# Performance work log

Measured on AMD Instinct MI355X. Metric: run time of the kernel, lower is better.

Reference implementation:

```python
import jax, jax.numpy as jnp
import numpy as np

B, S, K, D, H, F = 2, 2048, 2048, 1024, 16, 4096
HD = D // H
LN_EPS = 1e-5  # nn.LayerNorm default (module's eps arg is unused by the norms)


def setup_inputs() -> dict:
    key = jax.random.key(0)
    ks = jax.random.split(key, 12)
    def w(k, shape, scale=0.02):
        return jax.random.normal(k, shape, jnp.float32) * scale
    return {
        "x": jax.random.normal(ks[0], (B, S, D), jnp.float32),
        "context": jax.random.normal(ks[1], (B, K, D), jnp.float32),
        "Wq": w(ks[2], (D, D)), "bq": jnp.zeros((D,), jnp.float32),
        "Wk": w(ks[3], (D, D)), "bk": jnp.zeros((D,), jnp.float32),
        "Wv": w(ks[4], (D, D)), "bv": jnp.zeros((D,), jnp.float32),
        "W1": w(ks[5], (F, D)), "b1": jnp.zeros((F,), jnp.float32),
        "W2": w(ks[6], (D, F)), "b2": jnp.zeros((D,), jnp.float32),
        "g1": jnp.ones((D,), jnp.float32), "be1": jnp.zeros((D,), jnp.float32),
        "g2": jnp.ones((D,), jnp.float32), "be2": jnp.zeros((D,), jnp.float32),
    }


def _ln(x, g, b):
    m = jnp.mean(x, axis=-1, keepdims=True)
    v = jnp.var(x, axis=-1, keepdims=True)
    return (x - m) / jnp.sqrt(v + LN_EPS) * g + b


def _split_heads(t, L):
    # [B, L, D] -> [B, H, L, HD]
    return t.reshape(B, L, H, HD).transpose(0, 2, 1, 3)


def reference(x, context, Wq, bq, Wk, bk, Wv, bv, W1, b1, W2, b2, g1, be1, g2, be2):
    q = _split_heads(x @ Wq.T + bq, S)
    k = _split_heads(context @ Wk.T + bk, K)
    v = _split_heads(context @ Wv.T + bv, K)
    # NOTE: original scales by sqrt(encoder_out_dim), not sqrt(head_dim)
    scores = jnp.einsum('bhqd,bhkd->bhqk', q, k) / jnp.sqrt(jnp.float32(D))
    attn = jax.nn.softmax(scores, axis=-1)
    ctx = jnp.einsum('bhqk,bhkd->bhqd', attn, v)
    # faithful to original: raw reshape of [B,H,S,HD] -> [B,S,D] (no head transpose)
    out1 = ctx.reshape(B, S, D)
    out1 = x + _ln(out1, g1, be1)
    h = jax.nn.gelu(out1 @ W1.T + b1, approximate=False)
    out2 = _ln(h @ W2.T + b2, g2, be2)
    return out1 + out2
```

## Files before the change

kernel.cpp:

```cpp
#include <hip/hip_runtime.h>
#include <hip/hip_bf16.h>

#define BB 2
#define SS 2048
#define KK 2048
#define DD 1024
#define HH 16
#define FF 4096

using bf16x8 = __attribute__((ext_vector_type(8))) __bf16;
using f32x4  = __attribute__((ext_vector_type(4))) float;
using u16 = unsigned short;

__device__ __forceinline__ float bf2f(u16 u){
  union { unsigned int i; float f; } c; c.i = ((unsigned int)u) << 16; return c.f;
}
__device__ __forceinline__ u16 f2bf(float f){
  union { float f; unsigned int i; } c; c.f = f;
  return (u16)((c.i + 0x7fffu + ((c.i >> 16) & 1u)) >> 16);
}
__device__ __forceinline__ float gelu_exact(float x){
  return 0.5f * x * (1.f + erff(x * 0.70710678118654752f));
}

__device__ __forceinline__ void gll16(const void* g, const void* l) {
  __builtin_amdgcn_global_load_lds(
      (const __attribute__((address_space(1))) void*)(unsigned long long)(size_t)g,
      (__attribute__((address_space(3))) void*)(unsigned int)(size_t)l,
      16, 0, 0);
}

#define E_X   0
#define E_CX  4194304
#define E_WQ  8388608
#define E_BQ  9437184
#define E_WK  9438208
#define E_BK  10486784
#define E_WV  10487808
#define E_BV  11536384
#define E_W1  11537408
#define E_B1  15731712
#define E_W2  15735808
#define E_B2  19930112
#define E_G1  19931136
#define E_BE1 19932160
#define E_G2  19933184
#define E_BE2 19934208
#define E_TOT 19935232

struct Ptrs { const void* p[16]; };

__global__ __launch_bounds__(256)
void convert_inputs(Ptrs ptrs, u16* __restrict__ dst)
{
  const bool is_f32 = (((const u16*)ptrs.p[12])[0] == 0);
  const int szs[16] = {4194304, 4194304, 1048576, 1024, 1048576, 1024,
                       1048576, 1024, 4194304, 4096, 4194304, 1024,
                       1024, 1024, 1024, 1024};
  long long gbase = (long long)blockIdx.x * 1024;
  int seg = 0; long long start = 0;
  while (seg < 15 && gbase >= start + szs[seg]) { start += szs[seg]; seg++; }
  const long long local = gbase - start;
  const int tid = threadIdx.x;
  u16 outv[4];
  if (is_f32) {
    const float4* s = (const float4*)((const float*)ptrs.p[seg] + local);
    float4 v = s[tid];
    outv[0] = f2bf(v.x); outv[1] = f2bf(v.y); outv[2] = f2bf(v.z); outv[3] = f2bf(v.w);
  } else {
    const uint2* s = (const uint2*)((const u16*)ptrs.p[seg] + local);
    uint2 v = s[tid];
    *(uint2*)outv = v;
  }
  *(uint2*)(dst + gbase + (long long)tid * 4) = *(uint2*)outv;
}

template<int EPI>
__device__ __forceinline__
void gemm256_core(const u16* __restrict__ A, const u16* __restrict__ W,
                  const u16* __restrict__ bias, void* __restrict__ Cout,
                  int N, int Kd, int lda, int n0, int m0, u16* lds)
{
  const int tid = threadIdx.x;
  const int wv = tid >> 6, lane = tid & 63;
  const int wm = wv >> 2, wn = wv & 3;
  const int l16 = lane & 15, quad = lane >> 4;
  const int sw = (quad ^ ((l16 >> 1) & 3)) * 8;

  const int aRdOff = (wm * 128 + l16) * 32 + sw;
  const int bRdOff = (wn * 64 + l16) * 32 + sw;

  const int rA0 = wm * 128 + wn * 32 + (lane >> 2);
  const int rB0 = (wn >> 1) * 128 + (wm * 2 + (wn & 1)) * 32 + (lane >> 2);
  const u16* gA = A + (size_t)(m0 + rA0) * lda + (((lane & 3) ^ ((rA0 >> 1) & 3)) * 8);
  const u16* gB = W + (size_t)(n0 + rB0) * lda + (((lane & 3) ^ ((rB0 >> 1) & 3)) * 8);
  const int aStBase = (wm * 128 + wn * 32) * 32;
  const int bStBase = ((wn >> 1) * 128 + (wm * 2 + (wn & 1)) * 32) * 32;
  const size_t rs16 = (size_t)16 * lda;

  f32x4 acc[8][4] = {};

  auto stage4 = [&](int nbo, int kc, int ktn) {
    const u16* ga = gA + ktn + kc * 32;
    const u16* gb = gB + ktn + kc * 32;
    u16* la = lds + nbo + kc * 8192 + aStBase;
    u16* lb = lds + nbo + 16384 + kc * 8192 + bStBase;
    gll16(ga, la); gll16(ga + rs16, la + 512);
    gll16(gb, lb); gll16(gb + rs16, lb + 512);
  };

  auto interval = [&](int bo, int nbo, int kc, int ktn) {
    asm volatile("s_waitcnt vmcnt(4)" ::: "memory");
    __builtin_amdgcn_s_barrier();
    asm volatile("" ::: "memory");
    stage4(nbo, kc, ktn);
    const u16* Ab = lds + bo + kc * 8192;
    const u16* Bb = Ab + 16384;
    bf16x8 bfr[4], afr[4];
#pragma unroll
    for (int j = 0; j < 4; ++j) bfr[j] = *(const bf16x8*)(Bb + bRdOff + j * 512);
#pragma unroll
    for (int i = 0; i < 4; ++i) afr[i] = *(const bf16x8*)(Ab + aRdOff + i * 512);
    __builtin_amdgcn_s_setprio(1);
#pragma unroll
    for (int i = 0; i < 4; ++i)
#pragma unroll
      for (int j = 0; j < 4; ++j)
        acc[i][j] = __builtin_amdgcn_mfma_f32_16x16x32_bf16(afr[i], bfr[j], acc[i][j], 0, 0, 0);
    __builtin_amdgcn_s_setprio(0);
#pragma unroll
    for (int i = 0; i < 4; ++i) afr[i] = *(const bf16x8*)(Ab + aRdOff + (4 + i) * 512);
    __builtin_amdgcn_s_setprio(1);
#pragma unroll
    for (int i = 0; i < 4; ++i)
#pragma unroll
      for (int j = 0; j < 4; ++j)
        acc[4 + i][j] = __builtin_amdgcn_mfma_f32_16x16x32_bf16(afr[i], bfr[j], acc[4 + i][j], 0, 0, 0);
    __builtin_amdgcn_s_setprio(0);
  };

  stage4(0, 0, 0);
  stage4(0, 1, 0);

  const int NT = Kd >> 6;
#pragma unroll 1
  for (int t = 0; t < NT; t += 2) {
    const int kt1 = ((t + 1 < NT) ? t + 1 : t) << 6;
    interval(0, 32768, 0, kt1);
    interval(0, 32768, 1, kt1);
    const int kt2 = ((t + 2 < NT) ? t + 2 : t + 1) << 6;
    interval(32768, 0, 0, kt2);
    interval(32768, 0, 1, kt2);
  }

#pragma unroll
  for (int i = 0; i < 8; i++)
#pragma unroll
    for (int j = 0; j < 4; j++) {
      const int mb = m0 + wm * 128 + 16 * i + quad * 4;
      const int n  = n0 + wn * 64 + 16 * j + l16;
      if (EPI == 5) {
#pragma unroll
        for (int r = 0; r < 4; r++)
          ((u16*)Cout)[(size_t)(mb + r) * N + n] = f2bf(acc[i][j][r]);
      } else {
        const float bv = bf2f(bias[n]);
        if (EPI == 3) {
          u16 pk[4];
#pragma unroll
          for (int r = 0; r < 4; r++) pk[r] = f2bf(acc[i][j][r] + bv);
          const int b = mb >> 11, key = mb & 2047;
          *(uint2*)((u16*)Cout + ((size_t)((b * HH + (n >> 6)) * 64 + (n & 63))) * KK + key)
              = *(uint2*)pk;
        } else {
#pragma unroll
          for (int r = 0; r < 4; r++) {
            float vv = acc[i][j][r] + bv;
            if (EPI == 1) vv = gelu_exact(vv);
            ((u16*)Cout)[(size_t)(mb + r) * N + n] = f2bf(vv);
          }
        }
      }
    }
}

template<int EPI>
__global__ __launch_bounds__(512, 2)
void gemm256(const u16* __restrict__ A, const u16* __restrict__ W,
             const u16* __restrict__ bias, void* __restrict__ Cout,
             int N, int Kd, int lda)
{
  __shared__ u16 lds[65536];
  gemm256_core<EPI>(A, W, bias, Cout, N, Kd, lda,
                    blockIdx.x * 256, blockIdx.y * 256, lds);
}

__global__ __launch_bounds__(512, 2)
void qkv_gemm256(const u16* __restrict__ conv, u16* __restrict__ q_ws,
                 u16* __restrict__ k_ws, u16* __restrict__ vt_ws)
{
  __shared__ u16 lds[65536];
  const int n0 = blockIdx.x * 256, m0 = blockIdx.y * 256;
  const int z = blockIdx.z;
  if (z == 0)
    gemm256_core<0>(conv + E_X,  conv + E_WQ, conv + E_BQ, q_ws,  DD, DD, DD, n0, m0, lds);
  else if (z == 1)
    gemm256_core<0>(conv + E_CX, conv + E_WK, conv + E_BK, k_ws,  DD, DD, DD, n0, m0, lds);
  else
    gemm256_core<3>(conv + E_CX, conv + E_WV, conv + E_BV, vt_ws, DD, DD, DD, n0, m0, lds);
}

__global__ __launch_bounds__(512, 2)
void ffn2_gemm256(const u16* __restrict__ h, const u16* __restrict__ W2,
                  u16* __restrict__ pa, u16* __restrict__ pb,
                  u16* __restrict__ pc, u16* __restrict__ pd)
{
  __shared__ u16 lds[65536];
  u16* outs[4] = {pa, pb, pc, pd};
  const int z = blockIdx.z;
  gemm256_core<5>(h + (size_t)z * 1024, W2 + (size_t)z * 1024, nullptr, outs[z],
                  DD, 1024, FF, blockIdx.x * 256, blockIdx.y * 256, lds);
}

#define ATT_SCALE 0.03125f

__global__ __launch_bounds__(512, 4)
void attn_flash(const u16* __restrict__ q, const u16* __restrict__ k,
                const u16* __restrict__ vt, const u16* __restrict__ x,
                const u16* __restrict__ g1, const u16* __restrict__ be1,
                u16* __restrict__ o1)
{
  __shared__ u16 Qs[128 * 64];
  __shared__ u16 Ks0[64 * 64], Ks1[64 * 64];
  __shared__ u16 Vt0[64 * 64], Vt1[64 * 64];
  __shared__ u16 Ps[8][16 * 72];
  const int tid = threadIdx.x, wv = tid >> 6, lane = tid & 63;
  const int l16 = lane & 15, quad = lane >> 4;
  const int s0 = blockIdx.x * 128;
  const int bh = blockIdx.y, b = bh >> 4, h = bh & 15;
  const size_t qgbase = ((size_t)b * SS + s0) * DD + h * 64;
  const size_t kgbase = (size_t)b * KK * DD + h * 64;
  const size_t vtbase = (size_t)bh * 64 * KK;
  const int srow = tid >> 3, sc8 = tid & 7;
  const int c8s = sc8 ^ (srow & 7);

  auto stage_kv = [&](u16* Ks, u16* Vt, int kt) {
    gll16(k + kgbase + (size_t)(kt + srow) * DD + c8s * 8, Ks + tid * 8);
    gll16(vt + vtbase + (size_t)srow * KK + kt + c8s * 8, Vt + tid * 8);
  };

#pragma unroll
  for (int n = 0; n < 2; n++) {
    int row = srow + 64 * n, c8 = sc8 ^ (row & 7);
    gll16(q + qgbase + (size_t)row * DD + c8 * 8, Qs + n * 4096 + tid * 8);
  }
  stage_kv(Ks0, Vt0, 0);
  stage_kv(Ks1, Vt1, 64);
  __syncthreads();

  bf16x8 qf[2];
#pragma unroll
  for (int kc = 0; kc < 2; kc++)
    qf[kc] = *(const bf16x8*)(Qs + (wv * 16 + l16) * 64
                              + (((kc << 2) | quad) ^ (l16 & 7)) * 8);

  f32x4 O[4] = {};
  float psum = 0.f;
  u16* Psw = Ps[wv];

  auto compute = [&](const u16* Ks, const u16* Vt) {
    bf16x8 bvf[4][2];
#pragma unroll
    for (int db = 0; db < 4; db++)
#pragma unroll
      for (int kc = 0; kc < 2; kc++)
        bvf[db][kc] = *(const bf16x8*)(Vt + (db * 16 + l16) * 64
                                       + (((kc << 2) | quad) ^ (l16 & 7)) * 8);
    uint2 pk2[4];
#pragma unroll
    for (int jj = 0; jj < 4; jj++) {
      f32x4 c = {};
      __builtin_amdgcn_s_setprio(1);
#pragma unroll
      for (int kc = 0; kc < 2; kc++) {
        bf16x8 ak = *(const bf16x8*)(Ks + (jj * 16 + l16) * 64
                                     + (((kc << 2) | quad) ^ (l16 & 7)) * 8);
        c = __builtin_amdgcn_mfma_f32_16x16x32_bf16(ak, qf[kc], c, 0, 0, 0);
      }
      __builtin_amdgcn_s_setprio(0);
      float p0 = __expf(c[0] * ATT_SCALE);
      float p1 = __expf(c[1] * ATT_SCALE);
      float p2 = __expf(c[2] * ATT_SCALE);
      float p3 = __expf(c[3] * ATT_SCALE);
      psum += (p0 + p1) + (p2 + p3);
      union { float f; unsigned u; } u0{p0}, u1{p1}, u2{p2}, u3{p3};
      pk2[jj].x = __builtin_amdgcn_perm(u1.u, u0.u, 0x07060302u);
      pk2[jj].y = __builtin_amdgcn_perm(u3.u, u2.u, 0x07060302u);
    }
#pragma unroll
    for (int jj = 0; jj < 4; jj++)
      *(uint2*)(Psw + l16 * 72 + jj * 16 + quad * 4) = pk2[jj];
    asm volatile("s_waitcnt lgkmcnt(0)" ::: "memory");
    bf16x8 pf[2];
#pragma unroll
    for (int kc = 0; kc < 2; kc++)
      pf[kc] = *(const bf16x8*)(Psw + l16 * 72 + kc * 32 + quad * 8);
    __builtin_amdgcn_s_setprio(1);
#pragma unroll
    for (int db = 0; db < 4; db++)
#pragma unroll
      for (int kc = 0; kc < 2; kc++)
        O[db] = __builtin_amdgcn_mfma_f32_16x16x32_bf16(pf[kc], bvf[db][kc], O[db], 0, 0, 0);
    __builtin_amdgcn_s_setprio(0);
  };

#pragma unroll 1
  for (int kt = 0; kt < KK - 128; kt += 128) {
    asm volatile("s_waitcnt vmcnt(2)" ::: "memory");
    __builtin_amdgcn_s_barrier();
    asm volatile("" ::: "memory");
    compute(Ks0, Vt0);
    asm volatile("" ::: "memory");
    __builtin_amdgcn_s_barrier();
    stage_kv(Ks0, Vt0, kt + 128);
    asm volatile("s_waitcnt vmcnt(2)" ::: "memory");
    __builtin_amdgcn_s_barrier();
    asm volatile("" ::: "memory");
    compute(Ks1, Vt1);
    asm volatile("" ::: "memory");
    __builtin_amdgcn_s_barrier();
    stage_kv(Ks1, Vt1, kt + 192);
  }
  asm volatile("s_waitcnt vmcnt(2)" ::: "memory");
  __builtin_amdgcn_s_barrier();
  asm volatile("" ::: "memory");
  compute(Ks0, Vt0);
  asm volatile("s_waitcnt vmcnt(0)" ::: "memory");
  __builtin_amdgcn_s_barrier();
  asm volatile("" ::: "memory");
  compute(Ks1, Vt1);

  float lf = psum;
  lf += __shfl_xor(lf, 16, 64);
  lf += __shfl_xor(lf, 32, 64);

  float v[4][4];
  float s = 0.f, s2 = 0.f;
#pragma unroll
  for (int r = 0; r < 4; r++) {
    float lv = __shfl(lf, quad * 4 + r, 64);
    float inv = 1.f / lv;
#pragma unroll
    for (int db = 0; db < 4; db++) {
      float t = O[db][r] * inv;
      v[db][r] = t;
      s += t; s2 += t * t;
    }
  }
#pragma unroll
  for (int off = 1; off < 64; off <<= 1) {
    s  += __shfl_xor(s,  off, 64);
    s2 += __shfl_xor(s2, off, 64);
  }
  const float mean = s * (1.f / 1024.f);
  const float rstd = rsqrtf(s2 * (1.f / 1024.f) - mean * mean + 1e-5f);
  const size_t base = ((size_t)(b * 2048 + h * 128 + (s0 >> 4) + wv)) << 10;
#pragma unroll
  for (int r = 0; r < 4; r++)
#pragma unroll
    for (int db = 0; db < 4; db++) {
      const int col = (quad * 4 + r) * 64 + db * 16 + l16;
      float nv = (v[db][r] - mean) * rstd * bf2f(g1[col]) + bf2f(be1[col]);
      o1[base + col] = f2bf(bf2f(x[base + col]) + nv);
    }
}

__global__ __launch_bounds__(256)
void ln2_res(const u16* __restrict__ pa, const u16* __restrict__ pb,
             const u16* __restrict__ pc, const u16* __restrict__ pd,
             const u16* __restrict__ b2, const u16* __restrict__ o1,
             const u16* __restrict__ g, const u16* __restrict__ be,
             const void* __restrict__ detect, void* __restrict__ out)
{
  const bool f32out = (((const u16*)detect)[0] == 0);
  const int row = blockIdx.x, tid = threadIdx.x;
  const size_t base = (size_t)row * 1024;
  float vv[4]; float s = 0.f, s2 = 0.f;
#pragma unroll
  for (int i = 0; i < 4; i++) {
    int col = tid + 256 * i;
    vv[i] = (bf2f(pa[base + col]) + bf2f(pb[base + col]))
          + (bf2f(pc[base + col]) + bf2f(pd[base + col])) + bf2f(b2[col]);
    s += vv[i]; s2 += vv[i] * vv[i];
  }
#pragma unroll
  for (int off = 32; off; off >>= 1) { s += __shfl_xor(s, off, 64); s2 += __shfl_xor(s2, off, 64); }
  __shared__ float red[2][4];
  const int wave = tid >> 6, lane = tid & 63;
  if (lane == 0) { red[0][wave] = s; red[1][wave] = s2; }
  __syncthreads();
  s  = red[0][0] + red[0][1] + red[0][2] + red[0][3];
  s2 = red[1][0] + red[1][1] + red[1][2] + red[1][3];
  const float mean = s * (1.f / 1024.f);
  const float rstd = rsqrtf(s2 * (1.f / 1024.f) - mean * mean + 1e-5f);
#pragma unroll
  for (int i = 0; i < 4; i++) {
    int col = tid + 256 * i;
    float nv = (vv[i] - mean) * rstd * bf2f(g[col]) + bf2f(be[col]);
    float res = bf2f(o1[base + col]) + nv;
    if (f32out) ((float*)out)[base + col] = res;
    else        ((u16*)out)[base + col]  = f2bf(res);
  }
}

extern "C" void kernel_launch(void* const* d_in, const int* in_sizes, int n_in,
                              void* d_out, int out_size, void* d_ws, size_t ws_size,
                              hipStream_t stream)
{
  char* ws = (char*)d_ws;
  const size_t MB = 1024 * 1024;
  u16* conv   = (u16*)ws;
  u16* q_ws   = (u16*)(ws + 40 * MB);
  u16* k_ws   = (u16*)(ws + 48 * MB);
  u16* vt_ws  = (u16*)(ws + 56 * MB);
  u16* o1_bf  = (u16*)(ws + 64 * MB);
  u16* pd     = (u16*)(ws + 72 * MB);
  u16* h_ws   = (u16*)(ws + 80 * MB);
  u16* pa     = q_ws;
  u16* pb     = k_ws;
  u16* pc     = vt_ws;

  Ptrs ptrs;
  for (int i = 0; i < 16; i++) ptrs.p[i] = d_in[i];

  dim3 blk(256), blk5(512);
  const int M = BB * SS;

  convert_inputs<<<dim3(E_TOT / 1024), blk, 0, stream>>>(ptrs, conv);

  qkv_gemm256<<<dim3(DD / 256, M / 256, 3), blk5, 0, stream>>>(conv, q_ws, k_ws, vt_ws);

  attn_flash<<<dim3(SS / 128, BB * HH), blk5, 0, stream>>>(
      q_ws, k_ws, vt_ws, conv + E_X, conv + E_G1, conv + E_BE1, o1_bf);

  gemm256<1><<<dim3(FF / 256, M / 256), blk5, 0, stream>>>(
      o1_bf, conv + E_W1, conv + E_B1, h_ws, FF, DD, DD);

  ffn2_gemm256<<<dim3(DD / 256, M / 256, 4), blk5, 0, stream>>>(
      h_ws, conv + E_W2, pa, pb, pc, pd);

  ln2_res<<<dim3(M), blk, 0, stream>>>(pa, pb, pc, pd, conv + E_B2, o1_bf,
                                       conv + E_G2, conv + E_BE2, d_in[12], d_out);
}
```

Baseline: 318.9 us.

## Interleave fine-grained LDS staging with register-double-buffered MFMA phases in GEMM loop

Rewrites the GEMM main loop into an eight-phase schedule per two K-tiles. A and B global-to-LDS loads are issued separately and spread across phases, and A/B fragments are double-buffered in registers so LDS reads for the next MFMA block overlap the current one. The goal is to hide LDS read latency and spread global-load issue more evenly around the matrix math. In exchange the loop has many more workgroup barriers and higher register pressure from the extra fragment buffers.

```diff
diff --git a/kernel.cpp b/kernel.cpp
--- a/kernel.cpp
+++ b/kernel.cpp
@@ -99,59 +99,76 @@
   const size_t rs16 = (size_t)16 * lda;
 
   f32x4 acc[8][4] = {};
-
-  auto stage4 = [&](int nbo, int kc, int ktn) {
+  bf16x8 af0[4], af1[4], bf0[4], bf1[4];
+
+  auto stgA = [&](int bo, int kc, int ktn) {
     const u16* ga = gA + ktn + kc * 32;
+    u16* la = lds + bo + kc * 8192 + aStBase;
+    gll16(ga, la); gll16(ga + rs16, la + 512);
+  };
+  auto stgB = [&](int bo, int kc, int ktn) {
     const u16* gb = gB + ktn + kc * 32;
-    u16* la = lds + nbo + kc * 8192 + aStBase;
-    u16* lb = lds + nbo + 16384 + kc * 8192 + bStBase;
-    gll16(ga, la); gll16(ga + rs16, la + 512);
+    u16* lb = lds + bo + 16384 + kc * 8192 + bStBase;
     gll16(gb, lb); gll16(gb + rs16, lb + 512);
   };
-
-  auto interval = [&](int bo, int nbo, int kc, int ktn) {
-    asm volatile("s_waitcnt vmcnt(4)" ::: "memory");
-    __builtin_amdgcn_s_barrier();
-    asm volatile("" ::: "memory");
-    stage4(nbo, kc, ktn);
-    const u16* Ab = lds + bo + kc * 8192;
-    const u16* Bb = Ab + 16384;
-    bf16x8 bfr[4], afr[4];
-#pragma unroll
-    for (int j = 0; j < 4; ++j) bfr[j] = *(const bf16x8*)(Bb + bRdOff + j * 512);
-#pragma unroll
-    for (int i = 0; i < 4; ++i) afr[i] = *(const bf16x8*)(Ab + aRdOff + i * 512);
+  auto rdA = [&](bf16x8 (&d)[4], int bo, int kc, int h) {
+    const u16* p = lds + bo + kc * 8192 + aRdOff + h * 2048;
+#pragma unroll
+    for (int i = 0; i < 4; ++i) d[i] = *(const bf16x8*)(p + i * 512);
+  };
+  auto rdB = [&](bf16x8 (&d)[4], int bo, int kc) {
+    const u16* p = lds + bo + 16384 + kc * 8192 + bRdOff;
+#pragma unroll
+    for (int j = 0; j < 4; ++j) d[j] = *(const bf16x8*)(p + j * 512);
+  };
+  auto mma16 = [&](int h, const bf16x8 (&a)[4], const bf16x8 (&b)[4]) {
     __builtin_amdgcn_s_setprio(1);
 #pragma unroll
     for (int i = 0; i < 4; ++i)
 #pragma unroll
       for (int j = 0; j < 4; ++j)
-        acc[i][j] = __builtin_amdgcn_mfma_f32_16x16x32_bf16(afr[i], bfr[j], acc[i][j], 0, 0, 0);
+        acc[h * 4 + i][j] =
+            __builtin_amdgcn_mfma_f32_16x16x32_bf16(a[i], b[j], acc[h * 4 + i][j], 0, 0, 0);
     __builtin_amdgcn_s_setprio(0);
-#pragma unroll
-    for (int i = 0; i < 4; ++i) afr[i] = *(const bf16x8*)(Ab + aRdOff + (4 + i) * 512);
-    __builtin_amdgcn_s_setprio(1);
-#pragma unroll
-    for (int i = 0; i < 4; ++i)
-#pragma unroll
-      for (int j = 0; j < 4; ++j)
-        acc[4 + i][j] = __builtin_amdgcn_mfma_f32_16x16x32_bf16(afr[i], bfr[j], acc[4 + i][j], 0, 0, 0);
-    __builtin_amdgcn_s_setprio(0);
-  };
-
-  stage4(0, 0, 0);
-  stage4(0, 1, 0);
+  };
+#define BAR()  __builtin_amdgcn_s_barrier()
+#define VMC2() asm volatile("s_waitcnt vmcnt(2)" ::: "memory")
+
+  stgA(0, 0, 0); stgB(0, 0, 0); stgA(0, 1, 0); stgB(0, 1, 0);
+  asm volatile("s_waitcnt vmcnt(0)" ::: "memory");
+  BAR();
+  rdA(af0, 0, 0, 0);
+  rdB(bf0, 0, 0);
 
   const int NT = Kd >> 6;
 #pragma unroll 1
   for (int t = 0; t < NT; t += 2) {
-    const int kt1 = ((t + 1 < NT) ? t + 1 : t) << 6;
-    interval(0, 32768, 0, kt1);
-    interval(0, 32768, 1, kt1);
-    const int kt2 = ((t + 2 < NT) ? t + 2 : t + 1) << 6;
-    interval(32768, 0, 0, kt2);
-    interval(32768, 0, 1, kt2);
-  }
+    const int kB = (t + 1) << 6;
+    const int kN = (t + 2) << 6;
+    const bool more = (t + 2) < NT;
+    stgA(32768, 0, kB); rdA(af1, 0, 0, 1); VMC2(); BAR();
+    mma16(0, af0, bf0); BAR();
+    stgB(32768, 0, kB); rdA(af0, 0, 1, 0); rdB(bf1, 0, 1); BAR();
+    mma16(1, af1, bf0); BAR();
+    stgA(32768, 1, kB); rdA(af1, 0, 1, 1); VMC2(); BAR();
+    mma16(0, af0, bf1); BAR();
+    stgB(32768, 1, kB); rdA(af0, 32768, 0, 0); rdB(bf0, 32768, 0); BAR();
+    mma16(1, af1, bf1); BAR();
+    if (more) stgA(0, 0, kN);
+    rdA(af1, 32768, 0, 1); VMC2(); BAR();
+    mma16(0, af0, bf0); BAR();
+    if (more) stgB(0, 0, kN);
+    rdA(af0, 32768, 1, 0); rdB(bf1, 32768, 1); BAR();
+    mma16(1, af1, bf0); BAR();
+    if (more) stgA(0, 1, kN);
+    rdA(af1, 32768, 1, 1); VMC2(); BAR();
+    mma16(0, af0, bf1); BAR();
+    if (more) stgB(0, 1, kN);
+    rdA(af0, 0, 0, 0); rdB(bf0, 0, 0); BAR();
+    mma16(1, af1, bf1); BAR();
+  }
+#undef BAR
+#undef VMC2
 
 #pragma unroll
   for (int i = 0; i < 8; i++)
```

Result: slower. 425.1 us (+33.3%).
